# Performance work log

Measured on AMD Instinct MI355X. Metric: run time of the kernel, lower is better.

## Reference

```python
import jax, jax.numpy as jnp
from jax import lax
import numpy as np

B, T, V, H = 64, 256, 4096, 512


def setup_inputs() -> dict:
    key = jax.random.key(0)
    k1, k2, k3, k4 = jax.random.split(key, 4)
    x = jax.random.randint(k1, (B, T), 0, V, dtype=jnp.int32)
    # RNNScratch params (std=0.01 normal init, as in the LM head)
    Wxh = 0.01 * jax.random.normal(k2, (V, H), dtype=jnp.float32)
    Whh = 0.01 * jax.random.normal(k3, (H, H), dtype=jnp.float32)
    bh = jnp.zeros((H,), dtype=jnp.float32)
    Wo = 0.01 * jax.random.normal(k4, (H, V), dtype=jnp.float32)
    Bo = jnp.zeros((V,), dtype=jnp.float32)
    return {"x": x, "Wxh": Wxh, "Whh": Whh, "bh": bh, "Wo": Wo, "Bo": Bo}


def reference(x, Wxh, Whh, bh, Wo, Bo):
    # one_hot(x).float() @ Wxh is exactly a row gather from Wxh
    xs = jnp.take(Wxh, x.T, axis=0)  # [T, B, H]
    h0 = jnp.zeros((x.shape[0], Whh.shape[0]), dtype=Wxh.dtype)

    def step(h, xt):
        h = jnp.tanh(xt + h @ Whh + bh)  # [B, H]
        return h, h

    _, hs = lax.scan(step, h0, xs)  # hs: [T, B, H]
    # per-step output projection, fused into one einsum over time
    out = jnp.einsum("tbh,hv->btv", hs, Wo) + Bo  # [B, T, V]
    return out
```

## Files before the change

kernel.cpp:

```cpp
#include <hip/hip_runtime.h>


typedef __fp16 half2_t __attribute__((ext_vector_type(2)));
typedef __attribute__((ext_vector_type(8))) short short8;
typedef __attribute__((ext_vector_type(4))) float f32x4;

__device__ __forceinline__ unsigned short f32_to_bf16(float f) {
  unsigned int u = __builtin_bit_cast(unsigned int, f);
  u = (u + 0x7FFFu + ((u >> 16) & 1u)) >> 16;
  return (unsigned short)u;
}

__device__ __forceinline__ unsigned int pack_f16x2(float a, float b) {
  half2_t h = __builtin_amdgcn_cvt_pkrtz(a, b);
  return __builtin_bit_cast(unsigned int, h);
}

__device__ __forceinline__ float fdot2_(unsigned int w, unsigned int h, float acc) {
  return __builtin_amdgcn_fdot2(__builtin_bit_cast(half2_t, w),
                                __builtin_bit_cast(half2_t, h), acc, false);
}

__device__ __forceinline__ void glds16(const void* g, void* lds) {
  __builtin_amdgcn_global_load_lds(
      (const __attribute__((address_space(1))) unsigned int*)g,
      (__attribute__((address_space(3))) unsigned int*)lds, 16, 0, 0);
}

__global__ __launch_bounds__(256) void pack_whhB(const float* __restrict__ Whh,
                                                 unsigned int* __restrict__ WhhB,
                                                 unsigned long long* __restrict__ hG64) {
  int idx = blockIdx.x * 256 + threadIdx.x;
  int e = idx & 3;
  int G = idx >> 2;
  int c = G & 127;
  int u = (G >> 7) & 15;
  int q = (G >> 11) & 3;
  int s = G >> 13;
  int p = q * 64 + u * 4 + e;
  int j = s * 128 + c;
  float f0 = Whh[(2 * p) * 512 + j];
  float f1 = Whh[(2 * p + 1) * 512 + j];
  WhhB[idx] = pack_f16x2(f0, f1);
  if (idx < 32768) hG64[idx] = 0ull;
}

__global__ __launch_bounds__(256) void transpose_wo(const float* __restrict__ Wo,
                                                    unsigned short* __restrict__ WoT) {
  __shared__ float tile[64][65];
  const int tv = blockIdx.x;
  const int th = blockIdx.y;
  const int tid = threadIdx.x;
  const int c = tid & 63, r4 = tid >> 6;
#pragma unroll
  for (int p = 0; p < 16; ++p) {
    int hl = p * 4 + r4;
    tile[hl][c] = Wo[(size_t)(th * 64 + hl) * 4096 + tv * 64 + c];
  }
  __syncthreads();
#pragma unroll
  for (int p = 0; p < 16; ++p) {
    int vl = p * 4 + r4;
    WoT[(size_t)(tv * 64 + vl) * 512 + th * 64 + c] = f32_to_bf16(tile[c][vl]);
  }
}

#define DOTK(kc_, A) do { \
  const uint4 w_ = wlds[(kc_) * 128 + c]; \
  const uint4 h_ = hbuf[(kc_)]; \
  A = fdot2_(w_.x, h_.x, A); A = fdot2_(w_.y, h_.y, A); \
  A = fdot2_(w_.z, h_.z, A); A = fdot2_(w_.w, h_.w, A); } while (0)

__global__ __launch_bounds__(512) void rnn_scanD(const int* __restrict__ x,
                                                 const float* __restrict__ Wxh,
                                                 const unsigned int* __restrict__ WhhB,
                                                 const float* __restrict__ bh,
                                                 unsigned short* __restrict__ hs,
                                                 unsigned long long* hG64) {
  __shared__ uint4 wlds[8192];
  __shared__ uint4 hbuf[64];
  __shared__ float pbuf[512];
  __shared__ int toks[256];
  const int bid = blockIdx.x;
  const int s = bid & 3;
  const int b = bid >> 2;
  const int tid = threadIdx.x;
  const int c = tid & 127;
  const int q = tid >> 7;
  const int s16 = s * 16;
  const uint4* W4 = (const uint4*)WhhB;

#pragma unroll
  for (int it = 0; it < 16; ++it) {
    int L = it * 512 + tid;
    wlds[L] = W4[s * 8192 + L];
  }
  if (tid < 64) hbuf[tid] = make_uint4(0u, 0u, 0u, 0u);
  if (tid < 256) toks[tid] = x[b * 256 + tid];
  __syncthreads();

  unsigned int* hb32 = (unsigned int*)hbuf;
  const float bhj = (tid < 128) ? bh[s * 128 + tid] : 0.f;

  for (int t = 0; t < 256; ++t) {
    const int tok = toks[t];
    const float xv = (tid < 128) ? Wxh[(size_t)tok * 512 + s * 128 + tid] : 0.f;

    float a0 = 0.f, a1 = 0.f, a2 = 0.f, a3 = 0.f;
    DOTK(s16 + 0 + q, a0); DOTK(s16 + 4 + q, a1);
    DOTK(s16 + 8 + q, a2); DOTK(s16 + 12 + q, a3);

    if (t > 0 && tid < 192) {
      const int r = (tid < s * 64) ? tid : tid + 64;
      const unsigned long long* src =
          hG64 + (((size_t)(t & 1)) << 14) + b * 256 + r;
      unsigned long long v;
      do {
        v = __hip_atomic_load(src, __ATOMIC_RELAXED, __HIP_MEMORY_SCOPE_AGENT);
      } while ((unsigned)(v >> 32) != (unsigned)t);
      half2_t up = __builtin_bit_cast(half2_t, (unsigned)v);
      hb32[r] = pack_f16x2(tanhf((float)up.x), tanhf((float)up.y));
    }
    __syncthreads();

    {
      int m1 = ((s + 1) & 3) * 16;
      DOTK(m1 + 0 + q, a0); DOTK(m1 + 4 + q, a1);
      DOTK(m1 + 8 + q, a2); DOTK(m1 + 12 + q, a3);
      int m2 = ((s + 2) & 3) * 16;
      DOTK(m2 + 0 + q, a0); DOTK(m2 + 4 + q, a1);
      DOTK(m2 + 8 + q, a2); DOTK(m2 + 12 + q, a3);
      int m3 = ((s + 3) & 3) * 16;
      DOTK(m3 + 0 + q, a0); DOTK(m3 + 4 + q, a1);
      DOTK(m3 + 8 + q, a2); DOTK(m3 + 12 + q, a3);
    }
    pbuf[q * 128 + c] = (a0 + a1) + (a2 + a3);
    __syncthreads();

    if (tid < 128) {
      const float ssum = pbuf[tid] + pbuf[tid + 128] + pbuf[tid + 256] + pbuf[tid + 384];
      const float u1 = xv + ssum + bhj;
      const float u2 = __shfl_down(u1, 1);
      if (!(tid & 1)) {
        const unsigned int up = pack_f16x2(u1, u2);
        __hip_atomic_store(
            hG64 + (((size_t)((t + 1) & 1)) << 14) + b * 256 + 64 * s + (tid >> 1),
            ((unsigned long long)(unsigned)(t + 1) << 32) | up,
            __ATOMIC_RELAXED, __HIP_MEMORY_SCOPE_AGENT);
        half2_t uo = __builtin_bit_cast(half2_t, up);
        const float h1 = tanhf((float)uo.x);
        const float h2 = tanhf((float)uo.y);
        hb32[64 * s + (tid >> 1)] = pack_f16x2(h1, h2);
        ((unsigned int*)hs)[(size_t)(b * 256 + t) * 256 + 64 * s + (tid >> 1)] =
            (unsigned int)f32_to_bf16(h1) | ((unsigned int)f32_to_bf16(h2) << 16);
      }
    }
    __syncthreads();
  }
}

__global__ __launch_bounds__(256) void gemm_out(const unsigned short* __restrict__ A,
                                                const unsigned short* __restrict__ Bt,
                                                const float* __restrict__ Bo,
                                                float* __restrict__ C) {
  __shared__ alignas(16) unsigned short As[128 * 32];
  __shared__ alignas(16) unsigned short Bs[128 * 32];
  const int tid = threadIdx.x;
  const int lane = tid & 63, wid = tid >> 6;
  const int bn = blockIdx.x & 31, bm = blockIdx.x >> 5;
  const int wr = wid >> 1, wc = wid & 1;

  f32x4 acc[4][4] = {};

  const unsigned short* Ag = A + (size_t)(bm * 128 + (tid >> 2)) * 512 + (tid & 3) * 8;
  const unsigned short* Bg = Bt + (size_t)(bn * 128 + (tid >> 2)) * 512 + (tid & 3) * 8;
  char* AsW = (char*)As + wid * 1024;
  char* BsW = (char*)Bs + wid * 1024;

  const int laneRow = lane & 15;
  const int k0 = (lane >> 4) * 8;

  for (int kt = 0; kt < 16; ++kt) {
    __syncthreads();
    const unsigned short* a0 = Ag + kt * 32;
    const unsigned short* b0 = Bg + kt * 32;
    glds16(a0,            AsW);
    glds16(a0 + 64 * 512, AsW + 4096);
    glds16(b0,            BsW);
    glds16(b0 + 64 * 512, BsW + 4096);
    __syncthreads();

    short8 af[4], bf[4];
#pragma unroll
    for (int f = 0; f < 4; ++f)
      af[f] = *(const short8*)&As[(wr * 64 + f * 16 + laneRow) * 32 + k0];
#pragma unroll
    for (int f = 0; f < 4; ++f)
      bf[f] = *(const short8*)&Bs[(wc * 64 + f * 16 + laneRow) * 32 + k0];
#pragma unroll
    for (int fm = 0; fm < 4; ++fm)
#pragma unroll
      for (int fn = 0; fn < 4; ++fn)
        acc[fm][fn] = __builtin_amdgcn_mfma_f32_16x16x32_bf16(af[fm], bf[fn], acc[fm][fn], 0, 0, 0);
  }

  const int mg0 = bm * 128 + wr * 64, ng0 = bn * 128 + wc * 64;
#pragma unroll
  for (int fn = 0; fn < 4; ++fn) {
    const int col = ng0 + fn * 16 + laneRow;
    const float bo = Bo[col];
#pragma unroll
    for (int fm = 0; fm < 4; ++fm) {
      const int row0 = mg0 + fm * 16 + (lane >> 4) * 4;
#pragma unroll
      for (int r = 0; r < 4; ++r)
        C[(size_t)(row0 + r) * 4096 + col] = acc[fm][fn][r] + bo;
    }
  }
}

extern "C" void kernel_launch(void* const* d_in, const int* in_sizes, int n_in,
                              void* d_out, int out_size, void* d_ws, size_t ws_size,
                              hipStream_t stream) {
  (void)in_sizes; (void)n_in; (void)out_size; (void)ws_size;
  const int* x = (const int*)d_in[0];
  const float* Wxh = (const float*)d_in[1];
  const float* Whh = (const float*)d_in[2];
  const float* bh = (const float*)d_in[3];
  const float* Wo = (const float*)d_in[4];
  const float* Bo = (const float*)d_in[5];
  float* out = (float*)d_out;

  unsigned int* WhhB = (unsigned int*)d_ws;
  unsigned short* WoT = (unsigned short*)((char*)d_ws + 524288);
  unsigned short* hs = (unsigned short*)((char*)d_ws + 4718592);
  unsigned long long* hG64 = (unsigned long long*)((char*)d_ws + 21495808);

  hipLaunchKernelGGL(pack_whhB, dim3(512), dim3(256), 0, stream, Whh, WhhB, hG64);
  hipLaunchKernelGGL(transpose_wo, dim3(64, 8), dim3(256), 0, stream, Wo, WoT);
  hipLaunchKernelGGL(rnn_scanD, dim3(256), dim3(512), 0, stream, x, Wxh, WhhB, bh,
                     hs, hG64);
  hipLaunchKernelGGL(gemm_out, dim3(4096), dim3(256), 0, stream, hs, WoT, Bo, out);
}
```

Before: 518.0 us.

## Reduce RNN partial sums with wave shuffles and swizzle GEMM block order

Each output column now has its 4 K-partial sums held by 4 adjacent lanes and reduced with xor shuffles. This removes the pbuf LDS round-trip and one __syncthreads per timestep in the serial scan. It changes the LDS weight access pattern, since adjacent lanes now read different kc rows, which may raise bank conflicts. Separately, the output GEMM remaps block IDs with an XCD-style swizzle to improve L2 locality across the chiplets.

```diff
diff --git a/kernel.cpp b/kernel.cpp
--- a/kernel.cpp
+++ b/kernel.cpp
@@ -71,7 +71,7 @@
   A = fdot2_(w_.x, h_.x, A); A = fdot2_(w_.y, h_.y, A); \
   A = fdot2_(w_.z, h_.z, A); A = fdot2_(w_.w, h_.w, A); } while (0)
 
-__global__ __launch_bounds__(512) void rnn_scanD(const int* __restrict__ x,
+__global__ __launch_bounds__(512) void rnn_scanH(const int* __restrict__ x,
                                                  const float* __restrict__ Wxh,
                                                  const unsigned int* __restrict__ WhhB,
                                                  const float* __restrict__ bh,
@@ -79,14 +79,13 @@
                                                  unsigned long long* hG64) {
   __shared__ uint4 wlds[8192];
   __shared__ uint4 hbuf[64];
-  __shared__ float pbuf[512];
   __shared__ int toks[256];
   const int bid = blockIdx.x;
   const int s = bid & 3;
   const int b = bid >> 2;
   const int tid = threadIdx.x;
-  const int c = tid & 127;
-  const int q = tid >> 7;
+  const int c = tid >> 2;
+  const int q = tid & 3;
   const int s16 = s * 16;
   const uint4* W4 = (const uint4*)WhhB;
 
@@ -100,26 +99,26 @@
   __syncthreads();
 
   unsigned int* hb32 = (unsigned int*)hbuf;
-  const float bhj = (tid < 128) ? bh[s * 128 + tid] : 0.f;
+  const float bhj = bh[s * 128 + c];
+  const int rslot = (tid < s * 64) ? tid : tid + 64;
 
   for (int t = 0; t < 256; ++t) {
     const int tok = toks[t];
-    const float xv = (tid < 128) ? Wxh[(size_t)tok * 512 + s * 128 + tid] : 0.f;
+    const float xv = Wxh[(size_t)tok * 512 + s * 128 + c];
 
     float a0 = 0.f, a1 = 0.f, a2 = 0.f, a3 = 0.f;
     DOTK(s16 + 0 + q, a0); DOTK(s16 + 4 + q, a1);
     DOTK(s16 + 8 + q, a2); DOTK(s16 + 12 + q, a3);
 
     if (t > 0 && tid < 192) {
-      const int r = (tid < s * 64) ? tid : tid + 64;
       const unsigned long long* src =
-          hG64 + (((size_t)(t & 1)) << 14) + b * 256 + r;
+          hG64 + (((size_t)(t & 1)) << 14) + b * 256 + rslot;
       unsigned long long v;
       do {
         v = __hip_atomic_load(src, __ATOMIC_RELAXED, __HIP_MEMORY_SCOPE_AGENT);
       } while ((unsigned)(v >> 32) != (unsigned)t);
       half2_t up = __builtin_bit_cast(half2_t, (unsigned)v);
-      hb32[r] = pack_f16x2(tanhf((float)up.x), tanhf((float)up.y));
+      hb32[rslot] = pack_f16x2(tanhf((float)up.x), tanhf((float)up.y));
     }
     __syncthreads();
 
@@ -134,26 +133,24 @@
       DOTK(m3 + 0 + q, a0); DOTK(m3 + 4 + q, a1);
       DOTK(m3 + 8 + q, a2); DOTK(m3 + 12 + q, a3);
     }
-    pbuf[q * 128 + c] = (a0 + a1) + (a2 + a3);
-    __syncthreads();
-
-    if (tid < 128) {
-      const float ssum = pbuf[tid] + pbuf[tid + 128] + pbuf[tid + 256] + pbuf[tid + 384];
-      const float u1 = xv + ssum + bhj;
-      const float u2 = __shfl_down(u1, 1);
-      if (!(tid & 1)) {
-        const unsigned int up = pack_f16x2(u1, u2);
-        __hip_atomic_store(
-            hG64 + (((size_t)((t + 1) & 1)) << 14) + b * 256 + 64 * s + (tid >> 1),
-            ((unsigned long long)(unsigned)(t + 1) << 32) | up,
-            __ATOMIC_RELAXED, __HIP_MEMORY_SCOPE_AGENT);
-        half2_t uo = __builtin_bit_cast(half2_t, up);
-        const float h1 = tanhf((float)uo.x);
-        const float h2 = tanhf((float)uo.y);
-        hb32[64 * s + (tid >> 1)] = pack_f16x2(h1, h2);
-        ((unsigned int*)hs)[(size_t)(b * 256 + t) * 256 + 64 * s + (tid >> 1)] =
-            (unsigned int)f32_to_bf16(h1) | ((unsigned int)f32_to_bf16(h2) << 16);
-      }
+    float asum = (a0 + a1) + (a2 + a3);
+    asum += __shfl_xor(asum, 1);
+    asum += __shfl_xor(asum, 2);
+
+    const float u1 = xv + asum + bhj;
+    const float u2 = __shfl_down(u1, 4);
+    if ((tid & 7) == 0) {
+      const unsigned int up = pack_f16x2(u1, u2);
+      __hip_atomic_store(
+          hG64 + (((size_t)((t + 1) & 1)) << 14) + b * 256 + 64 * s + (tid >> 3),
+          ((unsigned long long)(unsigned)(t + 1) << 32) | up,
+          __ATOMIC_RELAXED, __HIP_MEMORY_SCOPE_AGENT);
+      half2_t uo = __builtin_bit_cast(half2_t, up);
+      const float h1 = tanhf((float)uo.x);
+      const float h2 = tanhf((float)uo.y);
+      hb32[64 * s + (tid >> 3)] = pack_f16x2(h1, h2);
+      ((unsigned int*)hs)[(size_t)(b * 256 + t) * 256 + 64 * s + (tid >> 3)] =
+          (unsigned int)f32_to_bf16(h1) | ((unsigned int)f32_to_bf16(h2) << 16);
     }
     __syncthreads();
   }
@@ -167,7 +164,8 @@
   __shared__ alignas(16) unsigned short Bs[128 * 32];
   const int tid = threadIdx.x;
   const int lane = tid & 63, wid = tid >> 6;
-  const int bn = blockIdx.x & 31, bm = blockIdx.x >> 5;
+  const int swz = (blockIdx.x & 7) * 512 + (blockIdx.x >> 3);
+  const int bn = swz & 31, bm = swz >> 5;
   const int wr = wid >> 1, wc = wid & 1;
 
   f32x4 acc[4][4] = {};
@@ -238,7 +236,7 @@
 
   hipLaunchKernelGGL(pack_whhB, dim3(512), dim3(256), 0, stream, Whh, WhhB, hG64);
   hipLaunchKernelGGL(transpose_wo, dim3(64, 8), dim3(256), 0, stream, Wo, WoT);
-  hipLaunchKernelGGL(rnn_scanD, dim3(256), dim3(512), 0, stream, x, Wxh, WhhB, bh,
+  hipLaunchKernelGGL(rnn_scanH, dim3(256), dim3(512), 0, stream, x, Wxh, WhhB, bh,
                      hs, hG64);
   hipLaunchKernelGGL(gemm_out, dim3(4096), dim3(256), 0, stream, hs, WoT, Bo, out);
 }
```

New measurement: 605.8 us. +16.9%, slower.
